# Kernel optimization log

Measured on AMD Instinct MI355X. Metric: run time of the kernel, lower is better.

## Reference

```python
import jax, jax.numpy as jnp
import numpy as np

NUM_LEAVES = 256
EPS = 1e-6
SHARPNESS = 1.0   # init_sharpness, non-trainable buffer
BIAS_SHIFT = -2.0


def _generalized_gcd(w1, w2, lambd):
    # lambd: per-node bias -> andness via sigmoid; broadcast over batch
    lam = jax.nn.sigmoid(lambd)
    a = jnp.abs(w1) + EPS
    b = jnp.abs(w2) + EPS
    return lam * jnp.minimum(a, b) + (1.0 - lam) * jnp.maximum(a, b)


def setup_inputs() -> dict:
    key = jax.random.key(0)
    ks = jax.random.split(key, 6)
    B, L = 65536, NUM_LEAVES
    x = jax.random.normal(ks[0], (B, L), jnp.float32)
    # xavier-like scale for the leaf projection
    W_leaf = jax.random.normal(ks[1], (L, L), jnp.float32) * (1.0 / np.sqrt(L))
    weights = jax.random.uniform(ks[2], (L - 1, 2), jnp.float32, 0.5, 1.5)
    biases = jax.random.uniform(ks[3], (L - 1,), jnp.float32) * 0.1
    w_out = jax.random.normal(ks[4], (1, 1), jnp.float32)
    b_out = jnp.full((1,), 0.5, jnp.float32)
    return {"x": x, "W_leaf": W_leaf, "weights": weights,
            "biases": biases, "w_out": w_out, "b_out": b_out}


def reference(x, W_leaf, weights, biases, w_out, b_out):
    # InputToLeafFC: sigmoid(sharpness * (x @ W^T + bias_shift))
    leaf = jax.nn.sigmoid(SHARPNESS * (x @ W_leaf.T + BIAS_SHIFT))  # (B, L)

    # The original pops two nodes from the front of the queue and appends the
    # result; for a power-of-two leaf count this is exactly a level-by-level
    # pairwise tree reduction, with node weights consumed in order.
    cur = leaf
    off = 0
    n = cur.shape[1]
    while n > 1:  # log2(L) levels, each fully vectorized over (batch, pairs)
        m = n // 2
        w = weights[off:off + m]   # (m, 2)
        b = biases[off:off + m]    # (m,)
        left = cur[:, 0::2] * w[:, 0]
        right = cur[:, 1::2] * w[:, 1]
        cur = _generalized_gcd(left, right, b)  # (B, m)
        off += m
        n = m
    # fc_out: Linear(1,1) then sigmoid -> (B, 1)
    return jax.nn.sigmoid(cur * w_out[0, 0] + b_out[0])
```

## Files before the change

kernel.cpp:

```cpp
#include <hip/hip_runtime.h>
#include <stdint.h>


#define EPS 1e-6f
#define LOG2E 1.44269504088896340736f

typedef __attribute__((ext_vector_type(8))) short short8;
typedef __attribute__((ext_vector_type(4))) short short4_t;
typedef __attribute__((ext_vector_type(4))) float float4_t;

__device__ __forceinline__ float fast_sigmoid(float z) {
    float e = __builtin_amdgcn_exp2f(-z * LOG2E);
    return __builtin_amdgcn_rcpf(1.0f + e);
}

__device__ __forceinline__ short f2bf(float f) {
    uint32_t u = __builtin_bit_cast(uint32_t, f);
    u += 0x7FFFu + ((u >> 16) & 1u);
    return (short)(u >> 16);
}

__device__ __forceinline__ short8 pack8(float4 a, float4 b) {
    short8 s;
    s[0] = f2bf(a.x); s[1] = f2bf(a.y); s[2] = f2bf(a.z); s[3] = f2bf(a.w);
    s[4] = f2bf(b.x); s[5] = f2bf(b.y); s[6] = f2bf(b.z); s[7] = f2bf(b.w);
    return s;
}

__device__ __forceinline__ float ggcd(float l, float r, float lam) {
    float a = fabsf(l) + EPS;
    float b = fabsf(r) + EPS;
    float mn = fminf(a, b);
    float mx = fmaxf(a, b);
    return fmaf(lam, mn - mx, mx);
}

__device__ __forceinline__ void tree_reduce(float4_t acc[16], int c0,
                                            const float4* pv, float res[4]) {
    #pragma unroll
    for (int t = 0; t < 16; ++t) {
        #pragma unroll
        for (int r = 0; r < 4; ++r) acc[t][r] = fast_sigmoid(acc[t][r] - 2.0f);
    }
    #pragma unroll
    for (int tp = 0; tp < 8; ++tp) {
        float4 p = pv[c0 * 8 + tp];
        #pragma unroll
        for (int r = 0; r < 4; ++r)
            acc[tp][r] = ggcd(acc[2*tp][r] * p.x, acc[2*tp+1][r] * p.y, p.z);
    }
    #pragma unroll
    for (int tp = 0; tp < 4; ++tp) {
        float4 p = pv[128 + c0 * 4 + tp];
        #pragma unroll
        for (int r = 0; r < 4; ++r)
            acc[tp][r] = ggcd(acc[2*tp][r] * p.x, acc[2*tp+1][r] * p.y, p.z);
    }
    #pragma unroll
    for (int tp = 0; tp < 2; ++tp) {
        float4 p = pv[192 + c0 * 2 + tp];
        #pragma unroll
        for (int r = 0; r < 4; ++r)
            acc[tp][r] = ggcd(acc[2*tp][r] * p.x, acc[2*tp+1][r] * p.y, p.z);
    }
    {
        float4 p = pv[224 + c0];
        #pragma unroll
        for (int r = 0; r < 4; ++r)
            res[r] = ggcd(acc[0][r] * p.x, acc[1][r] * p.y, p.z);
    }
}

__device__ __forceinline__ void tree_tail(float res[4], int c0, int q,
                                          const float4* pv, float wo, float bo,
                                          float* __restrict__ out, int rb) {
    const int offs[4] = {240, 248, 252, 254};
    #pragma unroll
    for (int k = 0; k < 4; ++k) {
        float4 p = pv[offs[k] + (c0 >> (k + 1))];
        bool isLeft = ((c0 >> k) & 1) == 0;
        #pragma unroll
        for (int r = 0; r < 4; ++r) {
            float other = __shfl_xor(res[r], 1 << k, 64);
            float lf = isLeft ? res[r] : other;
            float rt = isLeft ? other  : res[r];
            res[r] = ggcd(lf * p.x, rt * p.y, p.z);
        }
    }
    if (c0 == 0) {
        #pragma unroll
        for (int r = 0; r < 4; ++r)
            out[rb + q * 4 + r] = fast_sigmoid(fmaf(res[r], wo, bo));
    }
}

__global__ __launch_bounds__(512, 2)
void btln_main(const float* __restrict__ x, const float* __restrict__ Wl,
               const float* __restrict__ wts, const float* __restrict__ bia,
               const float* __restrict__ wout, const float* __restrict__ bout,
               float* __restrict__ out) {
    __shared__ short Wt[4][16384];
    __shared__ float4 pv[256];

    const int tid  = threadIdx.x;
    const int lane = tid & 63;
    const int wv   = tid >> 6;
    const int c0   = lane & 15;
    const int q    = lane >> 4;

    if (tid < 255) {
        pv[tid] = make_float4(wts[2 * tid], wts[2 * tid + 1],
                              fast_sigmoid(bia[tid]), 0.f);
    } else if (tid == 255) {
        pv[255] = make_float4(0.f, 0.f, 0.f, 0.f);
    }

    {
        const int scpos = tid & 7;
        const int sj    = tid >> 3;
        const int colx  = (scpos ^ (sj & 7)) << 3;
        #pragma unroll
        for (int half = 0; half < 4; ++half) {
            const int j   = sj + 64 * half;
            const int src = ((j & 15) << 4) | (j >> 4);
            #pragma unroll
            for (int kt = 0; kt < 4; ++kt) {
                const float* p = Wl + src * 256 + kt * 64 + colx;
                float4 a0 = *(const float4*)(p);
                float4 a1 = *(const float4*)(p + 4);
                *(short8*)((char*)&Wt[kt][0] + j * 128 + scpos * 16) = pack8(a0, a1);
            }
        }
    }

    const int rowbase = blockIdx.x * 256 + wv * 32;
    const float* xrA = x + (size_t)(rowbase + c0) * 256;
    const float* xrB = x + (size_t)(rowbase + 16 + c0) * 256;

    float4 r0 = *(const float4*)(xrA + q * 8);
    float4 r1 = *(const float4*)(xrA + q * 8 + 4);
    float4 r2 = *(const float4*)(xrA + 32 + q * 8);
    float4 r3 = *(const float4*)(xrA + 32 + q * 8 + 4);
    float4 s0 = *(const float4*)(xrB + q * 8);
    float4 s1 = *(const float4*)(xrB + q * 8 + 4);
    float4 s2 = *(const float4*)(xrB + 32 + q * 8);
    float4 s3 = *(const float4*)(xrB + 32 + q * 8 + 4);
    short8 afA0 = pack8(r0, r1);
    short8 afA1 = pack8(r2, r3);
    short8 afB0 = pack8(s0, s1);
    short8 afB1 = pack8(s2, s3);

    float4_t accA[16], accB[16];
    #pragma unroll
    for (int t = 0; t < 16; ++t) {
        accA[t] = (float4_t){0.f, 0.f, 0.f, 0.f};
        accB[t] = (float4_t){0.f, 0.f, 0.f, 0.f};
    }

    __syncthreads();

    const int vx = c0 & 7;

#define MFMA_T(t)                                                             \
    {                                                                         \
        const short* base = &cur[((t) * 16 + c0) * 64];                       \
        short8 bf0 = *(const short8*)&base[(q ^ vx) * 8];                     \
        short8 bf1 = *(const short8*)&base[((q + 4) ^ vx) * 8];               \
        accA[t] = __builtin_amdgcn_mfma_f32_16x16x32_bf16(                    \
            afA0, bf0, accA[t], 0, 0, 0);                                     \
        accA[t] = __builtin_amdgcn_mfma_f32_16x16x32_bf16(                    \
            afA1, bf1, accA[t], 0, 0, 0);                                     \
        accB[t] = __builtin_amdgcn_mfma_f32_16x16x32_bf16(                    \
            afB0, bf0, accB[t], 0, 0, 0);                                     \
        accB[t] = __builtin_amdgcn_mfma_f32_16x16x32_bf16(                    \
            afB1, bf1, accB[t], 0, 0, 0);                                     \
    }

#define KSTEP(kt, LAST)                                                       \
    {                                                                         \
        const short* cur = &Wt[kt][0];                                        \
        float4 n0, n1, n2, n3, m0, m1, m2, m3;                                \
        if (!(LAST)) {                          \
            const float* xnA = xrA + ((kt) + 1) * 64;                         \
            const float* xnB = xrB + ((kt) + 1) * 64;                         \
            n0 = *(const float4*)(xnA + q * 8);                               \
            n1 = *(const float4*)(xnA + q * 8 + 4);                           \
            n2 = *(const float4*)(xnA + 32 + q * 8);                          \
            n3 = *(const float4*)(xnA + 32 + q * 8 + 4);                      \
            m0 = *(const float4*)(xnB + q * 8);                               \
            m1 = *(const float4*)(xnB + q * 8 + 4);                           \
            m2 = *(const float4*)(xnB + 32 + q * 8);                          \
            m3 = *(const float4*)(xnB + 32 + q * 8 + 4);                      \
        }                                                                     \
        _Pragma("unroll")                                                     \
        for (int t = 0; t < 16; ++t) MFMA_T(t)                                \
        if (!(LAST)) {                                                        \
            afA0 = pack8(n0, n1);                                             \
            afA1 = pack8(n2, n3);                                             \
            afB0 = pack8(m0, m1);                                             \
            afB1 = pack8(m2, m3);                                             \
        }                                                                     \
        __builtin_amdgcn_sched_barrier(0);       \
    }

    KSTEP(0, 0)
    KSTEP(1, 0)
    KSTEP(2, 0)
    KSTEP(3, 1)
#undef KSTEP
#undef MFMA_T

    const float wo = wout[0];
    const float bo = bout[0];
    {
        float res[4];
        tree_reduce(accA, c0, pv, res);
        tree_tail(res, c0, q, pv, wo, bo, out, rowbase);
    }
    {
        float res[4];
        tree_reduce(accB, c0, pv, res);
        tree_tail(res, c0, q, pv, wo, bo, out, rowbase + 16);
    }
}

extern "C" void kernel_launch(void* const* d_in, const int* in_sizes, int n_in,
                              void* d_out, int out_size, void* d_ws, size_t ws_size,
                              hipStream_t stream) {
    const float* x   = (const float*)d_in[0];
    const float* Wl  = (const float*)d_in[1];
    const float* wts = (const float*)d_in[2];
    const float* bia = (const float*)d_in[3];
    const float* wo  = (const float*)d_in[4];
    const float* bo  = (const float*)d_in[5];
    float* out = (float*)d_out;

    const int rows = out_size;
    dim3 grid(rows / 256), block(512);
    btln_main<<<grid, block, 0, stream>>>(x, Wl, wts, bia, wo, bo, out);
}
```

Baseline: 113.9 us.

## Deepen x prefetch pipeline, use hardware bf16 pack, pad param LDS, vectorize output

```diff
diff --git a/kernel.cpp b/kernel.cpp
--- a/kernel.cpp
+++ b/kernel.cpp
@@ -6,7 +6,6 @@
 #define LOG2E 1.44269504088896340736f
 
 typedef __attribute__((ext_vector_type(8))) short short8;
-typedef __attribute__((ext_vector_type(4))) short short4_t;
 typedef __attribute__((ext_vector_type(4))) float float4_t;
 
 __device__ __forceinline__ float fast_sigmoid(float z) {
@@ -14,17 +13,15 @@
     return __builtin_amdgcn_rcpf(1.0f + e);
 }
 
-__device__ __forceinline__ short f2bf(float f) {
-    uint32_t u = __builtin_bit_cast(uint32_t, f);
-    u += 0x7FFFu + ((u >> 16) & 1u);
-    return (short)(u >> 16);
-}
-
 __device__ __forceinline__ short8 pack8(float4 a, float4 b) {
-    short8 s;
-    s[0] = f2bf(a.x); s[1] = f2bf(a.y); s[2] = f2bf(a.z); s[3] = f2bf(a.w);
-    s[4] = f2bf(b.x); s[5] = f2bf(b.y); s[6] = f2bf(b.z); s[7] = f2bf(b.w);
-    return s;
+    uint32_t u0, u1, u2, u3;
+    asm("v_cvt_pk_bf16_f32 %0, %1, %2" : "=v"(u0) : "v"(a.x), "v"(a.y));
+    asm("v_cvt_pk_bf16_f32 %0, %1, %2" : "=v"(u1) : "v"(a.z), "v"(a.w));
+    asm("v_cvt_pk_bf16_f32 %0, %1, %2" : "=v"(u2) : "v"(b.x), "v"(b.y));
+    asm("v_cvt_pk_bf16_f32 %0, %1, %2" : "=v"(u3) : "v"(b.z), "v"(b.w));
+    union { uint32_t u[4]; short8 s; } r;
+    r.u[0] = u0; r.u[1] = u1; r.u[2] = u2; r.u[3] = u3;
+    return r.s;
 }
 
 __device__ __forceinline__ float ggcd(float l, float r, float lam) {
@@ -35,6 +32,8 @@
     return fmaf(lam, mn - mx, mx);
 }
 
+__device__ __forceinline__ int pvIdx(int i) { return i + (i >> 3); }
+
 __device__ __forceinline__ void tree_reduce(float4_t acc[16], int c0,
                                             const float4* pv, float res[4]) {
     #pragma unroll
@@ -44,27 +43,27 @@
     }
     #pragma unroll
     for (int tp = 0; tp < 8; ++tp) {
-        float4 p = pv[c0 * 8 + tp];
+        float4 p = pv[pvIdx(c0 * 8 + tp)];
         #pragma unroll
         for (int r = 0; r < 4; ++r)
             acc[tp][r] = ggcd(acc[2*tp][r] * p.x, acc[2*tp+1][r] * p.y, p.z);
     }
     #pragma unroll
     for (int tp = 0; tp < 4; ++tp) {
-        float4 p = pv[128 + c0 * 4 + tp];
+        float4 p = pv[pvIdx(128 + c0 * 4 + tp)];
         #pragma unroll
         for (int r = 0; r < 4; ++r)
             acc[tp][r] = ggcd(acc[2*tp][r] * p.x, acc[2*tp+1][r] * p.y, p.z);
     }
     #pragma unroll
     for (int tp = 0; tp < 2; ++tp) {
-        float4 p = pv[192 + c0 * 2 + tp];
+        float4 p = pv[pvIdx(192 + c0 * 2 + tp)];
         #pragma unroll
         for (int r = 0; r < 4; ++r)
             acc[tp][r] = ggcd(acc[2*tp][r] * p.x, acc[2*tp+1][r] * p.y, p.z);
     }
     {
-        float4 p = pv[224 + c0];
+        float4 p = pv[pvIdx(224 + c0)];
         #pragma unroll
         for (int r = 0; r < 4; ++r)
             res[r] = ggcd(acc[0][r] * p.x, acc[1][r] * p.y, p.z);
@@ -77,7 +76,7 @@
     const int offs[4] = {240, 248, 252, 254};
     #pragma unroll
     for (int k = 0; k < 4; ++k) {
-        float4 p = pv[offs[k] + (c0 >> (k + 1))];
+        float4 p = pv[pvIdx(offs[k] + (c0 >> (k + 1)))];
         bool isLeft = ((c0 >> k) & 1) == 0;
         #pragma unroll
         for (int r = 0; r < 4; ++r) {
@@ -88,9 +87,12 @@
         }
     }
     if (c0 == 0) {
-        #pragma unroll
-        for (int r = 0; r < 4; ++r)
-            out[rb + q * 4 + r] = fast_sigmoid(fmaf(res[r], wo, bo));
+        float4 o;
+        o.x = fast_sigmoid(fmaf(res[0], wo, bo));
+        o.y = fast_sigmoid(fmaf(res[1], wo, bo));
+        o.z = fast_sigmoid(fmaf(res[2], wo, bo));
+        o.w = fast_sigmoid(fmaf(res[3], wo, bo));
+        *(float4*)&out[rb + q * 4] = o;
     }
 }
 
@@ -100,7 +102,7 @@
                const float* __restrict__ wout, const float* __restrict__ bout,
                float* __restrict__ out) {
     __shared__ short Wt[4][16384];
-    __shared__ float4 pv[256];
+    __shared__ float4 pv[288];
 
     const int tid  = threadIdx.x;
     const int lane = tid & 63;
@@ -108,11 +110,34 @@
     const int c0   = lane & 15;
     const int q    = lane >> 4;
 
+    const int rowbase = blockIdx.x * 256 + wv * 32;
+    const float* xrA = x + (size_t)(rowbase + c0) * 256;
+    const float* xrB = x + (size_t)(rowbase + 16 + c0) * 256;
+
+#define LOADX(s0,s1,s2,s3,s4,s5,s6,s7, koff)                                  \
+    s0 = *(const float4*)(xrA + (koff) + q * 8);                              \
+    s1 = *(const float4*)(xrA + (koff) + q * 8 + 4);                          \
+    s2 = *(const float4*)(xrA + (koff) + 32 + q * 8);                         \
+    s3 = *(const float4*)(xrA + (koff) + 32 + q * 8 + 4);                     \
+    s4 = *(const float4*)(xrB + (koff) + q * 8);                              \
+    s5 = *(const float4*)(xrB + (koff) + q * 8 + 4);                          \
+    s6 = *(const float4*)(xrB + (koff) + 32 + q * 8);                         \
+    s7 = *(const float4*)(xrB + (koff) + 32 + q * 8 + 4);
+
+#define PACKAF(A0,A1,B0,B1, s0,s1,s2,s3,s4,s5,s6,s7)                          \
+    A0 = pack8(s0, s1); A1 = pack8(s2, s3);                                   \
+    B0 = pack8(s4, s5); B1 = pack8(s6, s7);
+
+    float4 P0,P1,P2,P3,P4,P5,P6,P7;
+    float4 Q0,Q1,Q2,Q3,Q4,Q5,Q6,Q7;
+    LOADX(P0,P1,P2,P3,P4,P5,P6,P7, 0)
+    LOADX(Q0,Q1,Q2,Q3,Q4,Q5,Q6,Q7, 64)
+
     if (tid < 255) {
-        pv[tid] = make_float4(wts[2 * tid], wts[2 * tid + 1],
-                              fast_sigmoid(bia[tid]), 0.f);
+        pv[pvIdx(tid)] = make_float4(wts[2 * tid], wts[2 * tid + 1],
+                                     fast_sigmoid(bia[tid]), 0.f);
     } else if (tid == 255) {
-        pv[255] = make_float4(0.f, 0.f, 0.f, 0.f);
+        pv[pvIdx(255)] = make_float4(0.f, 0.f, 0.f, 0.f);
     }
 
     {
@@ -133,22 +158,9 @@
         }
     }
 
-    const int rowbase = blockIdx.x * 256 + wv * 32;
-    const float* xrA = x + (size_t)(rowbase + c0) * 256;
-    const float* xrB = x + (size_t)(rowbase + 16 + c0) * 256;
-
-    float4 r0 = *(const float4*)(xrA + q * 8);
-    float4 r1 = *(const float4*)(xrA + q * 8 + 4);
-    float4 r2 = *(const float4*)(xrA + 32 + q * 8);
-    float4 r3 = *(const float4*)(xrA + 32 + q * 8 + 4);
-    float4 s0 = *(const float4*)(xrB + q * 8);
-    float4 s1 = *(const float4*)(xrB + q * 8 + 4);
-    float4 s2 = *(const float4*)(xrB + 32 + q * 8);
-    float4 s3 = *(const float4*)(xrB + 32 + q * 8 + 4);
-    short8 afA0 = pack8(r0, r1);
-    short8 afA1 = pack8(r2, r3);
-    short8 afB0 = pack8(s0, s1);
-    short8 afB1 = pack8(s2, s3);
+    short8 aA0, aA1, aB0, aB1;
+    short8 bA0, bA1, bB0, bB1;
+    PACKAF(aA0,aA1,aB0,aB1, P0,P1,P2,P3,P4,P5,P6,P7)
 
     float4_t accA[16], accB[16];
     #pragma unroll
@@ -161,54 +173,44 @@
 
     const int vx = c0 & 7;
 
-#define MFMA_T(t)                                                             \
-    {                                                                         \
-        const short* base = &cur[((t) * 16 + c0) * 64];                       \
-        short8 bf0 = *(const short8*)&base[(q ^ vx) * 8];                     \
-        short8 bf1 = *(const short8*)&base[((q + 4) ^ vx) * 8];               \
-        accA[t] = __builtin_amdgcn_mfma_f32_16x16x32_bf16(                    \
-            afA0, bf0, accA[t], 0, 0, 0);                                     \
-        accA[t] = __builtin_amdgcn_mfma_f32_16x16x32_bf16(                    \
-            afA1, bf1, accA[t], 0, 0, 0);                                     \
-        accB[t] = __builtin_amdgcn_mfma_f32_16x16x32_bf16(                    \
-            afB0, bf0, accB[t], 0, 0, 0);                                     \
-        accB[t] = __builtin_amdgcn_mfma_f32_16x16x32_bf16(                    \
-            afB1, bf1, accB[t], 0, 0, 0);                                     \
-    }
-
-#define KSTEP(kt, LAST)                                                       \
+#define MFMA16(kt, A0,A1,B0,B1)                                               \
     {                                                                         \
         const short* cur = &Wt[kt][0];                                        \
-        float4 n0, n1, n2, n3, m0, m1, m2, m3;                                \
-        if (!(LAST)) {                          \
-            const float* xnA = xrA + ((kt) + 1) * 64;                         \
-            const float* xnB = xrB + ((kt) + 1) * 64;                         \
-            n0 = *(const float4*)(xnA + q * 8);                               \
-            n1 = *(const float4*)(xnA + q * 8 + 4);                           \
-            n2 = *(const float4*)(xnA + 32 + q * 8);                          \
-            n3 = *(const float4*)(xnA + 32 + q * 8 + 4);                      \
-            m0 = *(const float4*)(xnB + q * 8);                               \
-            m1 = *(const float4*)(xnB + q * 8 + 4);                           \
-            m2 = *(const float4*)(xnB + 32 + q * 8);                          \
-            m3 = *(const float4*)(xnB + 32 + q * 8 + 4);                      \
+        _Pragma("unroll")                                                     \
+        for (int t = 0; t < 16; ++t) {                                        \
+            const short* base = &cur[(t * 16 + c0) * 64];                     \
+            short8 bf0 = *(const short8*)&base[(q ^ vx) * 8];                 \
+            short8 bf1 = *(const short8*)&base[((q + 4) ^ vx) * 8];           \
+            accA[t] = __builtin_amdgcn_mfma_f32_16x16x32_bf16(                \
+                A0, bf0, accA[t], 0, 0, 0);                                   \
+            accA[t] = __builtin_amdgcn_mfma_f32_16x16x32_bf16(                \
+                A1, bf1, accA[t], 0, 0, 0);                                   \
+            accB[t] = __builtin_amdgcn_mfma_f32_16x16x32_bf16(                \
+                B0, bf0, accB[t], 0, 0, 0);                                   \
+            accB[t] = __builtin_amdgcn_mfma_f32_16x16x32_bf16(                \
+                B1, bf1, accB[t], 0, 0, 0);                                   \
         }                                                                     \
-        _Pragma("unroll")                                                     \
-        for (int t = 0; t < 16; ++t) MFMA_T(t)                                \
-        if (!(LAST)) {                                                        \
-            afA0 = pack8(n0, n1);                                             \
-            afA1 = pack8(n2, n3);                                             \
-            afB0 = pack8(m0, m1);                                             \
-            afB1 = pack8(m2, m3);                                             \
-        }                                                                     \
-        __builtin_amdgcn_sched_barrier(0);       \
-    }
-
-    KSTEP(0, 0)
-    KSTEP(1, 0)
-    KSTEP(2, 0)
-    KSTEP(3, 1)
-#undef KSTEP
-#undef MFMA_T
+    }
+
+    PACKAF(bA0,bA1,bB0,bB1, Q0,Q1,Q2,Q3,Q4,Q5,Q6,Q7)
+    LOADX(P0,P1,P2,P3,P4,P5,P6,P7, 128)
+    MFMA16(0, aA0,aA1,aB0,aB1)
+    __builtin_amdgcn_sched_barrier(0);
+
+    PACKAF(aA0,aA1,aB0,aB1, P0,P1,P2,P3,P4,P5,P6,P7)
+    LOADX(Q0,Q1,Q2,Q3,Q4,Q5,Q6,Q7, 192)
+    MFMA16(1, bA0,bA1,bB0,bB1)
+    __builtin_amdgcn_sched_barrier(0);
+
+    PACKAF(bA0,bA1,bB0,bB1, Q0,Q1,Q2,Q3,Q4,Q5,Q6,Q7)
+    MFMA16(2, aA0,aA1,aB0,aB1)
+    __builtin_amdgcn_sched_barrier(0);
+
+    MFMA16(3, bA0,bA1,bB0,bB1)
+
+#undef MFMA16
+#undef LOADX
+#undef PACKAF
 
     const float wo = wout[0];
     const float bo = bout[0];
```

After: 113.4 us. Within noise of the previous version (-0.4%).
